# Kernel optimization log

Measured on AMD Instinct MI355X. Metric: run time of the kernel, lower is better.

Reference implementation:

```python
import jax, jax.numpy as jnp
import numpy as np

B, H, S, D = 1, 16, 4096, 16

def setup_inputs() -> dict:
    key = jax.random.key(0)
    kq, kk, kv = jax.random.split(key, 3)
    q = jax.random.normal(kq, (B, H, S, D), dtype=jnp.float32)
    k = jax.random.normal(kk, (B, H, S, D), dtype=jnp.float32)
    v = jax.random.normal(kv, (B, H, S, D), dtype=jnp.float32)
    return {"q": q, "k": k, "v": v}

def reference(q, k, v):
    # Based linear attention: phi(s) = 1 + s + 0.5 s^2 on scaled scores,
    # causal mask, normalize by row-sum of feature-mapped scores.
    b, h, s, d = q.shape
    scale = 1.0 / np.sqrt(d)
    scores = jnp.einsum('bhqd,bhkd->bhqk', q * scale, k)   # [b,h,s,s]
    poly = 1.0 + scores + 0.5 * scores * scores
    causal = jnp.tril(jnp.ones((s, s), dtype=bool))        # j <= i
    poly = jnp.where(causal, poly, 0.0)
    z = jnp.sum(poly, axis=-1)                             # [b,h,s]
    out = jnp.einsum('bhqk,bhkd->bhqd', poly, v) / (z[..., None] + 1e-6)
    return out
```

## Files before the change

kernel.cpp:

```cpp
#include <hip/hip_runtime.h>


namespace {
constexpr int H = 16;
constexpr int S = 4096;
constexpr int D = 16;
constexpr int C = 128;
constexpr int NC = S / C;
constexpr int OFF_S2 = 0;
constexpr int OFF_S1 = 4096;
constexpr int OFF_Z2 = 4352;
constexpr int OFF_Z1 = 4608;
constexpr int OFF_V0 = 4624;
constexpr int STATE = 4640;
}

__global__ __launch_bounds__(256) void based_chunk_state(
    const float* __restrict__ kg_, const float* __restrict__ vg_,
    float* __restrict__ ws, int hb) {
  const int c = blockIdx.x;
  const int hl = blockIdx.y;
  const int h = hb + hl;
  const int tid = threadIdx.x;
  __shared__ float ks[C * D];
  __shared__ float vs[C * D];
  const float* kg = kg_ + ((size_t)h * S + (size_t)c * C) * D;
  const float* vg = vg_ + ((size_t)h * S + (size_t)c * C) * D;
#pragma unroll
  for (int i = 0; i < (C * D / 4) / 256; ++i) {
    int idx = tid + i * 256;
    reinterpret_cast<float4*>(ks)[idx] = reinterpret_cast<const float4*>(kg)[idx];
    reinterpret_cast<float4*>(vs)[idx] = reinterpret_cast<const float4*>(vg)[idx];
  }
  __syncthreads();

  const int d1 = tid >> 4;
  const int d2 = tid & 15;
  float s2a[16];
#pragma unroll
  for (int i = 0; i < 16; ++i) s2a[i] = 0.f;
  float z2a = 0.f, s1a = 0.f, z1a = 0.f, v0a = 0.f;

  for (int j = 0; j < C; ++j) {
    const float kd1 = ks[j * 16 + d1];
    const float kd2 = ks[j * 16 + d2];
    const float vd2 = vs[j * 16 + d2];
    const float w = kd1 * kd2;
    z2a += w;
    s1a = fmaf(kd1, vd2, s1a);
    v0a += vd2;
    z1a += kd1;
    const float4 va = *reinterpret_cast<const float4*>(&vs[j * 16 + 0]);
    const float4 vb = *reinterpret_cast<const float4*>(&vs[j * 16 + 4]);
    const float4 vc = *reinterpret_cast<const float4*>(&vs[j * 16 + 8]);
    const float4 vd = *reinterpret_cast<const float4*>(&vs[j * 16 + 12]);
    s2a[0]  = fmaf(w, va.x, s2a[0]);
    s2a[1]  = fmaf(w, va.y, s2a[1]);
    s2a[2]  = fmaf(w, va.z, s2a[2]);
    s2a[3]  = fmaf(w, va.w, s2a[3]);
    s2a[4]  = fmaf(w, vb.x, s2a[4]);
    s2a[5]  = fmaf(w, vb.y, s2a[5]);
    s2a[6]  = fmaf(w, vb.z, s2a[6]);
    s2a[7]  = fmaf(w, vb.w, s2a[7]);
    s2a[8]  = fmaf(w, vc.x, s2a[8]);
    s2a[9]  = fmaf(w, vc.y, s2a[9]);
    s2a[10] = fmaf(w, vc.z, s2a[10]);
    s2a[11] = fmaf(w, vc.w, s2a[11]);
    s2a[12] = fmaf(w, vd.x, s2a[12]);
    s2a[13] = fmaf(w, vd.y, s2a[13]);
    s2a[14] = fmaf(w, vd.z, s2a[14]);
    s2a[15] = fmaf(w, vd.w, s2a[15]);
  }

  float* st = ws + ((size_t)hl * NC + c) * STATE;
#pragma unroll
  for (int i = 0; i < 4; ++i) {
    float4 t = make_float4(s2a[4 * i + 0], s2a[4 * i + 1], s2a[4 * i + 2], s2a[4 * i + 3]);
    *reinterpret_cast<float4*>(&st[OFF_S2 + tid * 16 + 4 * i]) = t;
  }
  st[OFF_Z2 + tid] = z2a;
  st[OFF_S1 + tid] = s1a;
  if (d2 == 0) st[OFF_Z1 + d1] = z1a;
  if (d1 == 0) st[OFF_V0 + d2] = v0a;
}

__global__ __launch_bounds__(256) void based_scan(float* __restrict__ ws) {
  const int e = blockIdx.x * 256 + threadIdx.x;
  if (e >= STATE) return;
  const int hl = blockIdx.y;
  float* p = ws + (size_t)hl * NC * STATE + e;
  float vals[NC];
#pragma unroll
  for (int c = 0; c < NC; ++c) vals[c] = p[(size_t)c * STATE];
  float run = 0.f;
#pragma unroll
  for (int c = 0; c < NC; ++c) {
    const float t = vals[c];
    p[(size_t)c * STATE] = run;
    run += t;
  }
}

__device__ __forceinline__ float dot16(const float* __restrict__ qr,
                                       const float4 a, const float4 b,
                                       const float4 cc, const float4 d) {
  float s0 = fmaf(qr[0], a.x, qr[1] * a.y);
  s0 = fmaf(qr[2], a.z, s0);
  s0 = fmaf(qr[3], a.w, s0);
  float s1 = fmaf(qr[4], b.x, qr[5] * b.y);
  s1 = fmaf(qr[6], b.z, s1);
  s1 = fmaf(qr[7], b.w, s1);
  float s2 = fmaf(qr[8], cc.x, qr[9] * cc.y);
  s2 = fmaf(qr[10], cc.z, s2);
  s2 = fmaf(qr[11], cc.w, s2);
  float s3 = fmaf(qr[12], d.x, qr[13] * d.y);
  s3 = fmaf(qr[14], d.z, s3);
  s3 = fmaf(qr[15], d.w, s3);
  return (s0 + s1) + (s2 + s3);
}

__global__ __launch_bounds__(256) void based_out(
    const float* __restrict__ qg_, const float* __restrict__ kg_,
    const float* __restrict__ vg_, const float* __restrict__ ws,
    float* __restrict__ outg_, int hb) {
  const int c = blockIdx.x;
  const int hl = blockIdx.y;
  const int h = hb + hl;
  const int tid = threadIdx.x;
  __shared__ float qs[C * D];
  __shared__ float ksh[C * D];
  __shared__ float vsh[C * D];
  __shared__ float st[STATE];

  const float* qg = qg_ + ((size_t)h * S + (size_t)c * C) * D;
  const float* kg = kg_ + ((size_t)h * S + (size_t)c * C) * D;
  const float* vg = vg_ + ((size_t)h * S + (size_t)c * C) * D;
  const float* stg = ws + ((size_t)hl * NC + c) * STATE;

#pragma unroll
  for (int i = 0; i < (C * D / 4) / 256; ++i) {
    int idx = tid + i * 256;
    float4 t = reinterpret_cast<const float4*>(qg)[idx];
    t.x *= 0.25f; t.y *= 0.25f; t.z *= 0.25f; t.w *= 0.25f;
    reinterpret_cast<float4*>(qs)[idx] = t;
    reinterpret_cast<float4*>(ksh)[idx] = reinterpret_cast<const float4*>(kg)[idx];
    reinterpret_cast<float4*>(vsh)[idx] = reinterpret_cast<const float4*>(vg)[idx];
  }
  for (int i = tid; i < STATE / 4; i += 256) {
    reinterpret_cast<float4*>(st)[i] = reinterpret_cast<const float4*>(stg)[i];
  }
  __syncthreads();

  const int pr = tid >> 2;
  const int dvq = tid & 3;
  const int iA = pr;
  const int iB = C - 1 - pr;

  float qA[16], qB[16];
#pragma unroll
  for (int ii = 0; ii < 4; ++ii) {
    const float4 a = *reinterpret_cast<const float4*>(&qs[iA * 16 + 4 * ii]);
    qA[4 * ii + 0] = a.x; qA[4 * ii + 1] = a.y; qA[4 * ii + 2] = a.z; qA[4 * ii + 3] = a.w;
    const float4 b = *reinterpret_cast<const float4*>(&qs[iB * 16 + 4 * ii]);
    qB[4 * ii + 0] = b.x; qB[4 * ii + 1] = b.y; qB[4 * ii + 2] = b.z; qB[4 * ii + 3] = b.w;
  }

  float zA = (float)(c * C), zB = (float)(c * C);
  float4 yA = *reinterpret_cast<const float4*>(&st[OFF_V0 + dvq * 4]);
  float4 yB = yA;

  for (int d1 = 0; d1 < 16; ++d1) {
    const float aA = qs[iA * 16 + d1];
    const float aB = qs[iB * 16 + d1];
    const float4 s1v = *reinterpret_cast<const float4*>(&st[OFF_S1 + d1 * 16 + dvq * 4]);
    const float rz1 = st[OFF_Z1 + d1];
    yA.x = fmaf(aA, s1v.x, yA.x); yA.y = fmaf(aA, s1v.y, yA.y);
    yA.z = fmaf(aA, s1v.z, yA.z); yA.w = fmaf(aA, s1v.w, yA.w);
    zA = fmaf(aA, rz1, zA);
    yB.x = fmaf(aB, s1v.x, yB.x); yB.y = fmaf(aB, s1v.y, yB.y);
    yB.z = fmaf(aB, s1v.z, yB.z); yB.w = fmaf(aB, s1v.w, yB.w);
    zB = fmaf(aB, rz1, zB);
  }

  for (int d1 = 0; d1 < 16; ++d1) {
    const float ahA = 0.5f * qs[iA * 16 + d1];
    const float ahB = 0.5f * qs[iB * 16 + d1];
#pragma unroll
    for (int d2 = 0; d2 < 16; ++d2) {
      const int p = d1 * 16 + d2;
      const float4 s2v = *reinterpret_cast<const float4*>(&st[OFF_S2 + p * 16 + dvq * 4]);
      const float rz2 = st[OFF_Z2 + p];
      const float wA = ahA * qA[d2];
      const float wB = ahB * qB[d2];
      yA.x = fmaf(wA, s2v.x, yA.x); yA.y = fmaf(wA, s2v.y, yA.y);
      yA.z = fmaf(wA, s2v.z, yA.z); yA.w = fmaf(wA, s2v.w, yA.w);
      zA = fmaf(wA, rz2, zA);
      yB.x = fmaf(wB, s2v.x, yB.x); yB.y = fmaf(wB, s2v.y, yB.y);
      yB.z = fmaf(wB, s2v.z, yB.z); yB.w = fmaf(wB, s2v.w, yB.w);
      zB = fmaf(wB, rz2, zB);
    }
  }

  for (int j = 0; j <= pr; ++j) {
    const float4 k0 = *reinterpret_cast<const float4*>(&ksh[j * 16 + 0]);
    const float4 k1 = *reinterpret_cast<const float4*>(&ksh[j * 16 + 4]);
    const float4 k2 = *reinterpret_cast<const float4*>(&ksh[j * 16 + 8]);
    const float4 k3 = *reinterpret_cast<const float4*>(&ksh[j * 16 + 12]);
    const float4 vv = *reinterpret_cast<const float4*>(&vsh[j * 16 + dvq * 4]);
    const float sA = dot16(qA, k0, k1, k2, k3);
    const float sB = dot16(qB, k0, k1, k2, k3);
    const float pA = fmaf(sA, fmaf(0.5f, sA, 1.f), 1.f);
    const float pB = fmaf(sB, fmaf(0.5f, sB, 1.f), 1.f);
    yA.x = fmaf(pA, vv.x, yA.x); yA.y = fmaf(pA, vv.y, yA.y);
    yA.z = fmaf(pA, vv.z, yA.z); yA.w = fmaf(pA, vv.w, yA.w);
    zA += pA;
    yB.x = fmaf(pB, vv.x, yB.x); yB.y = fmaf(pB, vv.y, yB.y);
    yB.z = fmaf(pB, vv.z, yB.z); yB.w = fmaf(pB, vv.w, yB.w);
    zB += pB;
  }
  for (int j = pr + 1; j <= C - 1 - pr; ++j) {
    const float4 k0 = *reinterpret_cast<const float4*>(&ksh[j * 16 + 0]);
    const float4 k1 = *reinterpret_cast<const float4*>(&ksh[j * 16 + 4]);
    const float4 k2 = *reinterpret_cast<const float4*>(&ksh[j * 16 + 8]);
    const float4 k3 = *reinterpret_cast<const float4*>(&ksh[j * 16 + 12]);
    const float4 vv = *reinterpret_cast<const float4*>(&vsh[j * 16 + dvq * 4]);
    const float sB = dot16(qB, k0, k1, k2, k3);
    const float pB = fmaf(sB, fmaf(0.5f, sB, 1.f), 1.f);
    yB.x = fmaf(pB, vv.x, yB.x); yB.y = fmaf(pB, vv.y, yB.y);
    yB.z = fmaf(pB, vv.z, yB.z); yB.w = fmaf(pB, vv.w, yB.w);
    zB += pB;
  }

  float* outg = outg_ + ((size_t)h * S + (size_t)c * C) * D;
  const float invA = 1.0f / (zA + 1e-6f);
  const float invB = 1.0f / (zB + 1e-6f);
  float4 oA = make_float4(yA.x * invA, yA.y * invA, yA.z * invA, yA.w * invA);
  float4 oB = make_float4(yB.x * invB, yB.y * invB, yB.z * invB, yB.w * invB);
  reinterpret_cast<float4*>(outg)[iA * 4 + dvq] = oA;
  reinterpret_cast<float4*>(outg)[iB * 4 + dvq] = oB;
}

extern "C" void kernel_launch(void* const* d_in, const int* in_sizes, int n_in,
                              void* d_out, int out_size, void* d_ws, size_t ws_size,
                              hipStream_t stream) {
  (void)in_sizes; (void)n_in; (void)out_size;
  const float* q = (const float*)d_in[0];
  const float* k = (const float*)d_in[1];
  const float* v = (const float*)d_in[2];
  float* out = (float*)d_out;
  float* ws = (float*)d_ws;

  const size_t per_head = (size_t)NC * STATE * sizeof(float);
  int hp = (int)(ws_size / per_head);
  if (hp < 1) hp = 1;
  if (hp > H) hp = H;

  for (int hb = 0; hb < H; hb += hp) {
    const int hn = (H - hb < hp) ? (H - hb) : hp;
    hipLaunchKernelGGL(based_chunk_state, dim3(NC, hn), dim3(256), 0, stream,
                       k, v, ws, hb);
    hipLaunchKernelGGL(based_scan, dim3((STATE + 255) / 256, hn), dim3(256), 0,
                       stream, ws);
    hipLaunchKernelGGL(based_out, dim3(NC, hn), dim3(256), 0, stream,
                       q, k, v, ws, out, hb);
  }
}
```

Baseline: 113.3 us.

## Exploit symmetric quadratic state and split intra-chunk dot across lanes with DPP

Stores only the upper-triangular (d1<=d2) entries of the second-order state, cutting the state from 256 to 136 pairs. This shrinks workspace traffic, the scan and the state loads in the output kernel, and the off-diagonal terms take doubled weights. The intra-chunk score dot product is split across the four lanes of each row and reduced with DPP quad shuffles, replacing redundant 16-wide dots per thread. The state kernel also reads v rows from global instead of LDS, and loops are unrolled with q taken from registers. This relies on the DPP lane grouping matching dvq, and it costs more register and instruction work per lane.

```diff
diff --git a/kernel.cpp b/kernel.cpp
--- a/kernel.cpp
+++ b/kernel.cpp
@@ -7,12 +7,25 @@
 constexpr int D = 16;
 constexpr int C = 128;
 constexpr int NC = S / C;
+constexpr int NP = 136;
 constexpr int OFF_S2 = 0;
-constexpr int OFF_S1 = 4096;
-constexpr int OFF_Z2 = 4352;
-constexpr int OFF_Z1 = 4608;
-constexpr int OFF_V0 = 4624;
-constexpr int STATE = 4640;
+constexpr int OFF_S1 = NP * 16;
+constexpr int OFF_Z2 = OFF_S1 + 256;
+constexpr int OFF_Z1 = OFF_Z2 + NP;
+constexpr int OFF_V0 = OFF_Z1 + 16;
+constexpr int STATE  = OFF_V0 + 16;
+
+__device__ __forceinline__ constexpr int tri(int d1, int d2) {
+  return d1 * 16 + d2 - (d1 * (d1 + 1)) / 2;
+}
+
+__device__ __forceinline__ float qsum4(float x) {
+  int a = __builtin_amdgcn_mov_dpp(__float_as_int(x), 0xB1, 0xF, 0xF, true);
+  x += __int_as_float(a);
+  int b = __builtin_amdgcn_mov_dpp(__float_as_int(x), 0x4E, 0xF, 0xF, true);
+  x += __int_as_float(b);
+  return x;
+}
 }
 
 __global__ __launch_bounds__(256) void based_chunk_state(
@@ -27,7 +40,7 @@
   const float* kg = kg_ + ((size_t)h * S + (size_t)c * C) * D;
   const float* vg = vg_ + ((size_t)h * S + (size_t)c * C) * D;
 #pragma unroll
-  for (int i = 0; i < (C * D / 4) / 256; ++i) {
+  for (int i = 0; i < 2; ++i) {
     int idx = tid + i * 256;
     reinterpret_cast<float4*>(ks)[idx] = reinterpret_cast<const float4*>(kg)[idx];
     reinterpret_cast<float4*>(vs)[idx] = reinterpret_cast<const float4*>(vg)[idx];
@@ -41,19 +54,20 @@
   for (int i = 0; i < 16; ++i) s2a[i] = 0.f;
   float z2a = 0.f, s1a = 0.f, z1a = 0.f, v0a = 0.f;
 
+#pragma unroll 2
   for (int j = 0; j < C; ++j) {
+    const float4 va = *reinterpret_cast<const float4*>(vg + j * 16 + 0);
+    const float4 vb = *reinterpret_cast<const float4*>(vg + j * 16 + 4);
+    const float4 vc = *reinterpret_cast<const float4*>(vg + j * 16 + 8);
+    const float4 vd = *reinterpret_cast<const float4*>(vg + j * 16 + 12);
     const float kd1 = ks[j * 16 + d1];
     const float kd2 = ks[j * 16 + d2];
-    const float vd2 = vs[j * 16 + d2];
+    const float vd2l = vs[j * 16 + d2];
     const float w = kd1 * kd2;
     z2a += w;
-    s1a = fmaf(kd1, vd2, s1a);
-    v0a += vd2;
     z1a += kd1;
-    const float4 va = *reinterpret_cast<const float4*>(&vs[j * 16 + 0]);
-    const float4 vb = *reinterpret_cast<const float4*>(&vs[j * 16 + 4]);
-    const float4 vc = *reinterpret_cast<const float4*>(&vs[j * 16 + 8]);
-    const float4 vd = *reinterpret_cast<const float4*>(&vs[j * 16 + 12]);
+    v0a += vd2l;
+    s1a = fmaf(kd1, vd2l, s1a);
     s2a[0]  = fmaf(w, va.x, s2a[0]);
     s2a[1]  = fmaf(w, va.y, s2a[1]);
     s2a[2]  = fmaf(w, va.z, s2a[2]);
@@ -73,12 +87,15 @@
   }
 
   float* st = ws + ((size_t)hl * NC + c) * STATE;
-#pragma unroll
-  for (int i = 0; i < 4; ++i) {
-    float4 t = make_float4(s2a[4 * i + 0], s2a[4 * i + 1], s2a[4 * i + 2], s2a[4 * i + 3]);
-    *reinterpret_cast<float4*>(&st[OFF_S2 + tid * 16 + 4 * i]) = t;
-  }
-  st[OFF_Z2 + tid] = z2a;
+  if (d1 <= d2) {
+    const int t = d1 * 16 + d2 - (d1 * (d1 + 1)) / 2;
+#pragma unroll
+    for (int i = 0; i < 4; ++i) {
+      float4 tv = make_float4(s2a[4 * i + 0], s2a[4 * i + 1], s2a[4 * i + 2], s2a[4 * i + 3]);
+      *reinterpret_cast<float4*>(&st[OFF_S2 + t * 16 + 4 * i]) = tv;
+    }
+    st[OFF_Z2 + t] = z2a;
+  }
   st[OFF_S1 + tid] = s1a;
   if (d2 == 0) st[OFF_Z1 + d1] = z1a;
   if (d1 == 0) st[OFF_V0 + d2] = v0a;
@@ -99,24 +116,6 @@
     p[(size_t)c * STATE] = run;
     run += t;
   }
-}
-
-__device__ __forceinline__ float dot16(const float* __restrict__ qr,
-                                       const float4 a, const float4 b,
-                                       const float4 cc, const float4 d) {
-  float s0 = fmaf(qr[0], a.x, qr[1] * a.y);
-  s0 = fmaf(qr[2], a.z, s0);
-  s0 = fmaf(qr[3], a.w, s0);
-  float s1 = fmaf(qr[4], b.x, qr[5] * b.y);
-  s1 = fmaf(qr[6], b.z, s1);
-  s1 = fmaf(qr[7], b.w, s1);
-  float s2 = fmaf(qr[8], cc.x, qr[9] * cc.y);
-  s2 = fmaf(qr[10], cc.z, s2);
-  s2 = fmaf(qr[11], cc.w, s2);
-  float s3 = fmaf(qr[12], d.x, qr[13] * d.y);
-  s3 = fmaf(qr[14], d.z, s3);
-  s3 = fmaf(qr[15], d.w, s3);
-  return (s0 + s1) + (s2 + s3);
 }
 
 __global__ __launch_bounds__(256) void based_out(
@@ -138,7 +137,7 @@
   const float* stg = ws + ((size_t)hl * NC + c) * STATE;
 
 #pragma unroll
-  for (int i = 0; i < (C * D / 4) / 256; ++i) {
+  for (int i = 0; i < 2; ++i) {
     int idx = tid + i * 256;
     float4 t = reinterpret_cast<const float4*>(qg)[idx];
     t.x *= 0.25f; t.y *= 0.25f; t.z *= 0.25f; t.w *= 0.25f;
@@ -164,14 +163,23 @@
     const float4 b = *reinterpret_cast<const float4*>(&qs[iB * 16 + 4 * ii]);
     qB[4 * ii + 0] = b.x; qB[4 * ii + 1] = b.y; qB[4 * ii + 2] = b.z; qB[4 * ii + 3] = b.w;
   }
+  const float qa0 = qs[iA * 16 + dvq * 4 + 0];
+  const float qa1 = qs[iA * 16 + dvq * 4 + 1];
+  const float qa2 = qs[iA * 16 + dvq * 4 + 2];
+  const float qa3 = qs[iA * 16 + dvq * 4 + 3];
+  const float qb0 = qs[iB * 16 + dvq * 4 + 0];
+  const float qb1 = qs[iB * 16 + dvq * 4 + 1];
+  const float qb2 = qs[iB * 16 + dvq * 4 + 2];
+  const float qb3 = qs[iB * 16 + dvq * 4 + 3];
 
   float zA = (float)(c * C), zB = (float)(c * C);
   float4 yA = *reinterpret_cast<const float4*>(&st[OFF_V0 + dvq * 4]);
   float4 yB = yA;
 
+#pragma unroll
   for (int d1 = 0; d1 < 16; ++d1) {
-    const float aA = qs[iA * 16 + d1];
-    const float aB = qs[iB * 16 + d1];
+    const float aA = qA[d1];
+    const float aB = qB[d1];
     const float4 s1v = *reinterpret_cast<const float4*>(&st[OFF_S1 + d1 * 16 + dvq * 4]);
     const float rz1 = st[OFF_Z1 + d1];
     yA.x = fmaf(aA, s1v.x, yA.x); yA.y = fmaf(aA, s1v.y, yA.y);
@@ -182,16 +190,16 @@
     zB = fmaf(aB, rz1, zB);
   }
 
+#pragma unroll
   for (int d1 = 0; d1 < 16; ++d1) {
-    const float ahA = 0.5f * qs[iA * 16 + d1];
-    const float ahB = 0.5f * qs[iB * 16 + d1];
-#pragma unroll
-    for (int d2 = 0; d2 < 16; ++d2) {
-      const int p = d1 * 16 + d2;
-      const float4 s2v = *reinterpret_cast<const float4*>(&st[OFF_S2 + p * 16 + dvq * 4]);
-      const float rz2 = st[OFF_Z2 + p];
-      const float wA = ahA * qA[d2];
-      const float wB = ahB * qB[d2];
+    const float a1A = qA[d1];
+    const float a1B = qB[d1];
+    {
+      const int t = tri(d1, d1);
+      const float4 s2v = *reinterpret_cast<const float4*>(&st[OFF_S2 + t * 16 + dvq * 4]);
+      const float rz2 = st[OFF_Z2 + t];
+      const float wA = 0.5f * a1A * a1A;
+      const float wB = 0.5f * a1B * a1B;
       yA.x = fmaf(wA, s2v.x, yA.x); yA.y = fmaf(wA, s2v.y, yA.y);
       yA.z = fmaf(wA, s2v.z, yA.z); yA.w = fmaf(wA, s2v.w, yA.w);
       zA = fmaf(wA, rz2, zA);
@@ -199,16 +207,33 @@
       yB.z = fmaf(wB, s2v.z, yB.z); yB.w = fmaf(wB, s2v.w, yB.w);
       zB = fmaf(wB, rz2, zB);
     }
+#pragma unroll
+    for (int d2 = d1 + 1; d2 < 16; ++d2) {
+      const int t = tri(d1, d2);
+      const float4 s2v = *reinterpret_cast<const float4*>(&st[OFF_S2 + t * 16 + dvq * 4]);
+      const float rz2 = st[OFF_Z2 + t];
+      const float wA = a1A * qA[d2];
+      const float wB = a1B * qB[d2];
+      yA.x = fmaf(wA, s2v.x, yA.x); yA.y = fmaf(wA, s2v.y, yA.y);
+      yA.z = fmaf(wA, s2v.z, yA.z); yA.w = fmaf(wA, s2v.w, yA.w);
+      zA = fmaf(wA, rz2, zA);
+      yB.x = fmaf(wB, s2v.x, yB.x); yB.y = fmaf(wB, s2v.y, yB.y);
+      yB.z = fmaf(wB, s2v.z, yB.z); yB.w = fmaf(wB, s2v.w, yB.w);
+      zB = fmaf(wB, rz2, zB);
+    }
   }
 
   for (int j = 0; j <= pr; ++j) {
-    const float4 k0 = *reinterpret_cast<const float4*>(&ksh[j * 16 + 0]);
-    const float4 k1 = *reinterpret_cast<const float4*>(&ksh[j * 16 + 4]);
-    const float4 k2 = *reinterpret_cast<const float4*>(&ksh[j * 16 + 8]);
-    const float4 k3 = *reinterpret_cast<const float4*>(&ksh[j * 16 + 12]);
+    const float4 kq = *reinterpret_cast<const float4*>(&ksh[j * 16 + dvq * 4]);
     const float4 vv = *reinterpret_cast<const float4*>(&vsh[j * 16 + dvq * 4]);
-    const float sA = dot16(qA, k0, k1, k2, k3);
-    const float sB = dot16(qB, k0, k1, k2, k3);
+    float sA = fmaf(qa0, kq.x, qa1 * kq.y);
+    sA = fmaf(qa2, kq.z, sA);
+    sA = fmaf(qa3, kq.w, sA);
+    float sB = fmaf(qb0, kq.x, qb1 * kq.y);
+    sB = fmaf(qb2, kq.z, sB);
+    sB = fmaf(qb3, kq.w, sB);
+    sA = qsum4(sA);
+    sB = qsum4(sB);
     const float pA = fmaf(sA, fmaf(0.5f, sA, 1.f), 1.f);
     const float pB = fmaf(sB, fmaf(0.5f, sB, 1.f), 1.f);
     yA.x = fmaf(pA, vv.x, yA.x); yA.y = fmaf(pA, vv.y, yA.y);
@@ -219,12 +244,12 @@
     zB += pB;
   }
   for (int j = pr + 1; j <= C - 1 - pr; ++j) {
-    const float4 k0 = *reinterpret_cast<const float4*>(&ksh[j * 16 + 0]);
-    const float4 k1 = *reinterpret_cast<const float4*>(&ksh[j * 16 + 4]);
-    const float4 k2 = *reinterpret_cast<const float4*>(&ksh[j * 16 + 8]);
-    const float4 k3 = *reinterpret_cast<const float4*>(&ksh[j * 16 + 12]);
+    const float4 kq = *reinterpret_cast<const float4*>(&ksh[j * 16 + dvq * 4]);
     const float4 vv = *reinterpret_cast<const float4*>(&vsh[j * 16 + dvq * 4]);
-    const float sB = dot16(qB, k0, k1, k2, k3);
+    float sB = fmaf(qb0, kq.x, qb1 * kq.y);
+    sB = fmaf(qb2, kq.z, sB);
+    sB = fmaf(qb3, kq.w, sB);
+    sB = qsum4(sB);
     const float pB = fmaf(sB, fmaf(0.5f, sB, 1.f), 1.f);
     yB.x = fmaf(pB, vv.x, yB.x); yB.y = fmaf(pB, vv.y, yB.y);
     yB.z = fmaf(pB, vv.z, yB.z); yB.w = fmaf(pB, vv.w, yB.w);
```

After: 100.3 us. 1.13x faster.
